# Optimization experiments

Hardware: AMD Instinct MI355X
Metric: run time of the kernel (lower is better)

## Reference

```python
import jax, jax.numpy as jnp
import numpy as np
import math

EPS = 1e-6
P_MIN = 1e-3
P_MAX = 10.0
NUM_ITERS = 3
REG = 1.0
K = 64       # num_clusters
D = 128      # cluster_dim
TOKEN = 256  # token_dim
B, N, C = 8, 8192, 512


def _l2norm(t):
    return t / jnp.clip(jnp.linalg.norm(t, axis=-1, keepdims=True), 1e-12)


def _mlp(h, W1, b1, W2, b2):
    # torch Linear: y = h @ W.T + b ; dropout is identity at eval
    return jax.nn.relu(h @ W1.T + b1) @ W2.T + b2


def _log_otp_solver(log_a, log_b, M, num_iters, reg):
    M = M / reg
    u = jnp.zeros_like(log_a)
    v = jnp.zeros_like(log_b)
    for _ in range(num_iters):  # fixed small iteration count
        u = log_a - jax.scipy.special.logsumexp(M + v[:, None, :], axis=2)
        v = log_b - jax.scipy.special.logsumexp(M + u[:, :, None], axis=1)
    return M + u[:, :, None] + v[:, None, :]


def _get_matching_probs(S, dustbin_score, num_iters, reg):
    b, m, n = S.shape
    dust_row = jnp.broadcast_to(dustbin_score, (b, 1, n)).astype(S.dtype)
    S_aug = jnp.concatenate([S, dust_row], axis=1)  # [b, m+1, n]
    norm = -math.log(n + m)
    log_a = jnp.full((m + 1,), norm, dtype=S.dtype).at[-1].add(math.log(n - m))
    log_a = jnp.broadcast_to(log_a, (b, m + 1))
    log_b = jnp.full((b, n), norm, dtype=S.dtype)
    log_P = _log_otp_solver(log_a, log_b, S_aug, num_iters, reg)
    return log_P - norm


def setup_inputs() -> dict:
    key = jax.random.key(0)
    ks = jax.random.split(key, 8)
    x = jax.random.normal(ks[0], (B, N, C), dtype=jnp.float32)

    def lin(k, fin, fout):
        k1, k2 = jax.random.split(k)
        W = 0.02 * jax.random.normal(k1, (fout, fin), dtype=jnp.float32)
        b = 0.02 * jax.random.normal(k2, (fout,), dtype=jnp.float32)
        return W, b

    tW1, tb1 = lin(ks[1], C, 512)
    tW2, tb2 = lin(ks[2], 512, TOKEN)
    cW1, cb1 = lin(ks[3], C, 512)
    cW2, cb2 = lin(ks[4], 512, D)
    sW1, sb1 = lin(ks[5], C, 512)
    sW2, sb2 = lin(ks[6], 512, K)
    # GeM p param init so that softplus(w)+p_min == 3.0
    gem_w = jnp.array([math.log(math.exp(3.0 - P_MIN) - 1.0)], dtype=jnp.float32)
    dust_bin = jnp.array(1.0, dtype=jnp.float32)
    return dict(x=x, gem_w=gem_w, dust_bin=dust_bin,
                tW1=tW1, tb1=tb1, tW2=tW2, tb2=tb2,
                cW1=cW1, cb1=cb1, cW2=cW2, cb2=cb2,
                sW1=sW1, sb1=sb1, sW2=sW2, sb2=sb2)


def reference(x, gem_w, dust_bin,
              tW1, tb1, tW2, tb2,
              cW1, cb1, cW2, cb2,
              sW1, sb1, sW2, sb2):
    # --- GeM pooling: [B, N, C] -> [B, C] ---
    p = jnp.minimum(jax.nn.softplus(gem_w) + P_MIN, P_MAX)  # [1]
    g = jnp.mean(jnp.clip(x.astype(jnp.float32), EPS, None) ** p, axis=1) ** (1.0 / p)
    g = jnp.where(jnp.isfinite(g), g, jnp.zeros_like(g))

    global_token = _mlp(g, tW1, tb1, tW2, tb2)          # [B, TOKEN]
    local = _mlp(x, cW1, cb1, cW2, cb2)                 # [B, N, D]
    scores = _mlp(x, sW1, sb1, sW2, sb2)                # [B, N, K]

    S = scores.transpose(0, 2, 1)                       # [B, K, N]
    log_P = _get_matching_probs(S, dust_bin, NUM_ITERS, REG)  # [B, K+1, N]
    p_mat = jnp.exp(log_P)[:, :-1, :]                   # drop dustbin -> [B, K, N]

    # aggregated[b, d, k] = sum_n local[b, n, d] * p[b, k, n]  (no O(B*D*K*N) blowup)
    agg = jnp.einsum('bnd,bkn->bdk', local, p_mat).reshape(x.shape[0], -1)  # [B, D*K]

    result = jnp.concatenate([_l2norm(global_token), _l2norm(agg)], axis=-1)
    return _l2norm(result)
```

## Files before the change

kernel.cpp:

```cpp
#include <hip/hip_runtime.h>
#include <hip/hip_bf16.h>
#include <math.h>

#define BB   8
#define NN   8192
#define CC   512
#define DD   128
#define KK   64
#define TOK  256
#define MM   (BB*NN)

typedef unsigned short u16;
typedef __attribute__((ext_vector_type(8))) short short8;
typedef __attribute__((ext_vector_type(4))) float floatx4;

struct PtrSz { const void* p[15]; int sz[15]; };

__device__ __forceinline__ float bf2f(u16 v) {
    union { unsigned u; float f; } x; x.u = ((unsigned)v) << 16; return x.f;
}
__device__ __forceinline__ u16 f2bf(float f) {
    union { float f; unsigned u; } x; x.f = f;
    unsigned r = x.u + 0x7fffu + ((x.u >> 16) & 1u);
    return (u16)(r >> 16);
}
__device__ __forceinline__ float nat_exp2(float a) {
    float r; asm("v_exp_f32 %0, %1" : "=v"(r) : "v"(a)); return r;
}
__device__ __forceinline__ float nat_log2(float a) {
    float r; asm("v_log_f32 %0, %1" : "=v"(r) : "v"(a)); return r;
}
__device__ __forceinline__ void gload16(const void* g, void* l) {
    __builtin_amdgcn_global_load_lds(
        (const __attribute__((address_space(1))) void*)g,
        (__attribute__((address_space(3))) void*)l, 16, 0, 0);
}

__global__ __launch_bounds__(256)
void fill_sentinel(float* __restrict__ out, int n, float val) {
    int i = blockIdx.x*256 + threadIdx.x;
    if (i < n) out[i] = val;
}

__global__ __launch_bounds__(256)
void detect_all(PtrSz ps, int* __restrict__ flags) {
    int i = blockIdx.x;
    const u16* q = (const u16*)ps.p[i];
    int m = ps.sz[i] < 4096 ? ps.sz[i] : 4096;
    __shared__ int cnt;
    if (threadIdx.x == 0) cnt = 0;
    __syncthreads();
    int c = 0;
    for (int j = threadIdx.x; j < m; j += 256) {
        int e = (q[j] >> 7) & 0xFF;
        if (e < 90 || e > 165) c++;
    }
    atomicAdd(&cnt, c);
    __syncthreads();
    if (threadIdx.x == 0) flags[i] = (cnt * 8 > m) ? 1 : 0;
}

#define W_TW1 0
#define W_TB1 262144
#define W_TW2 262656
#define W_TB2 393728
#define W_CW1 393984
#define W_CB1 656128
#define W_CW2 656640
#define W_CB2 722176
#define W_SW1 722304
#define W_SB1 984448
#define W_SW2 984960
#define W_SB2 1017728
#define W_TOTAL 1017792

__global__ __launch_bounds__(256)
void conv_weights(PtrSz ps, const int* __restrict__ flags,
                  u16* __restrict__ wbuf, float* __restrict__ wscal) {
    long gid = (long)blockIdx.x*256 + threadIdx.x;
    if (gid == 0) {
        float vb = bf2f(((const u16*)ps.p[1])[0]);
        float vf = ((const float*)ps.p[1])[0];
        wscal[0] = (fabsf(vb - 2.94694f) < 0.2f) ? vb : vf;
    } else if (gid == 1) {
        float vb = bf2f(((const u16*)ps.p[2])[0]);
        float vf = ((const float*)ps.p[2])[0];
        wscal[1] = (fabsf(vb - 1.0f) < 0.2f) ? vb : vf;
    }
    if (gid >= W_TOTAL) return;
    int idx; long off;
    if      (gid < W_TB1) { idx = 3;  off = W_TW1; }
    else if (gid < W_TW2) { idx = 4;  off = W_TB1; }
    else if (gid < W_TB2) { idx = 5;  off = W_TW2; }
    else if (gid < W_CW1) { idx = 6;  off = W_TB2; }
    else if (gid < W_CB1) { idx = 7;  off = W_CW1; }
    else if (gid < W_CW2) { idx = 8;  off = W_CB1; }
    else if (gid < W_CB2) { idx = 9;  off = W_CW2; }
    else if (gid < W_SW1) { idx = 10; off = W_CB2; }
    else if (gid < W_SB1) { idx = 11; off = W_SW1; }
    else if (gid < W_SW2) { idx = 12; off = W_SB1; }
    else if (gid < W_SB2) { idx = 13; off = W_SW2; }
    else                  { idx = 14; off = W_SB2; }
    long k = gid - off;
    bool f32in = flags[idx] != 0;
    wbuf[gid] = f32in ? f2bf(((const float*)ps.p[idx])[k]) : ((const u16*)ps.p[idx])[k];
}

__global__ __launch_bounds__(256)
void gem_partial(const void* __restrict__ x, const float* __restrict__ wscal,
                 const int* __restrict__ flags, float* __restrict__ gacc) {
    __shared__ float red[4][512];
    int b = blockIdx.x, ny = blockIdx.y;
    int tid  = threadIdx.x;
    int wave = tid >> 6, lane = tid & 63;
    bool f32in = (flags[0] != 0);
    float gw = wscal[0];
    float p  = fminf(log1pf(expf(gw)) + 1e-3f, 10.0f);
    int c0 = lane*8;
    float s[8];
#pragma unroll
    for (int j = 0; j < 8; ++j) s[j] = 0.f;
    size_t base = ((size_t)b*NN + (size_t)ny*64 + wave)*CC + c0;
    if (f32in) {
        const float* xf = (const float*)x;
#pragma unroll 4
        for (int n = 0; n < 64; n += 4) {
            const float* pf = xf + base + (size_t)n*CC;
            float4 x0 = *(const float4*)pf;
            float4 x1 = *(const float4*)(pf + 4);
            float xv[8] = {x0.x,x0.y,x0.z,x0.w,x1.x,x1.y,x1.z,x1.w};
#pragma unroll
            for (int j = 0; j < 8; ++j)
                s[j] += nat_exp2(p * nat_log2(fmaxf(xv[j], 1e-6f)));
        }
    } else {
        const u16* xu = (const u16*)x;
#pragma unroll 4
        for (int n = 0; n < 64; n += 4) {
            short8 v8 = *(const short8*)(xu + base + (size_t)n*CC);
#pragma unroll
            for (int j = 0; j < 8; ++j)
                s[j] += nat_exp2(p * nat_log2(fmaxf(bf2f((u16)v8[j]), 1e-6f)));
        }
    }
#pragma unroll
    for (int j = 0; j < 8; ++j) red[wave][c0 + j] = s[j];
    __syncthreads();
#pragma unroll
    for (int t = 0; t < 2; ++t) {
        int c = tid + t*256;
        float v = red[0][c] + red[1][c] + red[2][c] + red[3][c];
        atomicAdd(&gacc[b*CC + c], v);
    }
}

__global__ __launch_bounds__(256)
void gem_finalize(const float* __restrict__ gacc, const float* __restrict__ wscal,
                  float* __restrict__ g) {
    int i = blockIdx.x*256 + threadIdx.x;
    float gw = wscal[0];
    float p  = fminf(log1pf(expf(gw)) + 1e-3f, 10.0f);
    float m  = gacc[i] / (float)NN;
    float r  = powf(m, 1.0f/p);
    if (!isfinite(r)) r = 0.f;
    g[i] = r;
}

__global__ __launch_bounds__(512)
void token_mlp(const float* __restrict__ g, const u16* __restrict__ wbuf,
               float* __restrict__ t) {
    __shared__ float gs[CC];
    __shared__ float hs[512];
    int b = blockIdx.x, j = threadIdx.x;
    gs[j] = g[b*CC + j];
    __syncthreads();
    float a = bf2f(wbuf[W_TB1 + j]);
    const u16* w = wbuf + W_TW1 + (size_t)j*CC;
    for (int c = 0; c < CC; ++c) a += gs[c]*bf2f(w[c]);
    hs[j] = fmaxf(a, 0.f);
    __syncthreads();
    if (j < TOK) {
        float a2 = bf2f(wbuf[W_TB2 + j]);
        const u16* w2 = wbuf + W_TW2 + (size_t)j*512;
        for (int c = 0; c < 512; ++c) a2 += hs[c]*bf2f(w2[c]);
        t[b*TOK + j] = a2;
    }
}

template<int BN, int MODE, bool RELU, bool ARAW>
__global__ __launch_bounds__(256)
void gemm_bt(const void* __restrict__ A, const u16* __restrict__ W,
             const u16* __restrict__ bias, void* __restrict__ Cout,
             const int* __restrict__ flags, int N, int Ksz, int lda,
             size_t a_base, int bidx_ovr,
             const u16* __restrict__ W_alt, const u16* __restrict__ bias_alt,
             int nsplit) {
    constexpr int WSUB_N = BN/32;
    extern __shared__ char smem[];
    u16* a_lds = (u16*)smem;
    u16* b_lds = (u16*)smem + 128*32;
    const int tid  = threadIdx.x;
    const int wave = tid >> 6, lane = tid & 63;
    const int wm = wave >> 1, wn = wave & 1;

    int bx = blockIdx.x, by = blockIdx.y;
    {
        int nbx = gridDim.x, nby = gridDim.y;
        int nwg = nbx*nby;
        if ((nwg & 7) == 0) {
            int lid = bx + by*nbx;
            int q = nwg >> 3;
            int t = (lid & 7)*q + (lid >> 3);
            by = t % nby;
            bx = t / nby;
        }
    }
    const u16* Wp = W; const u16* bp = bias;
    int byw = by;
    if (W_alt != nullptr && by >= nsplit) { Wp = W_alt; bp = bias_alt; byw = by - nsplit; }
    const int bm0 = bx * 128;
    const int bn0 = by * BN;
    const int bw0 = byw * BN;
    const int fr = lane & 15;
    const int fk = (lane >> 4) * 8;
    const bool f32in = ARAW && (flags[0] != 0);

    floatx4 acc[4][WSUB_N];
#pragma unroll
    for (int i = 0; i < 4; ++i)
#pragma unroll
        for (int j = 0; j < WSUB_N; ++j) acc[i][j] = (floatx4){0.f,0.f,0.f,0.f};

    for (int k0 = 0; k0 < Ksz; k0 += 32) {
        if (f32in) {
#pragma unroll
            for (int part = 0; part < 2; ++part) {
                int chunk = part*256 + tid;
                int row = chunk >> 2, kc = (chunk & 3)*8;
                size_t gidx = a_base + (size_t)(bm0 + row)*lda + k0 + kc;
                const float* pf = (const float*)A + gidx;
                float4 x0 = *(const float4*)pf;
                float4 x1 = *(const float4*)(pf + 4);
                short8 vA;
                vA[0]=(short)f2bf(x0.x); vA[1]=(short)f2bf(x0.y);
                vA[2]=(short)f2bf(x0.z); vA[3]=(short)f2bf(x0.w);
                vA[4]=(short)f2bf(x1.x); vA[5]=(short)f2bf(x1.y);
                vA[6]=(short)f2bf(x1.z); vA[7]=(short)f2bf(x1.w);
                *(short8*)(a_lds + row*32 + kc) = vA;
            }
        } else {
#pragma unroll
            for (int part = 0; part < 2; ++part) {
                int cb = part*256 + wave*64;
                int mych = cb + lane;
                int row = mych >> 2, kc = (mych & 3)*8;
                gload16((const u16*)A + a_base + (size_t)(bm0 + row)*lda + k0 + kc,
                        a_lds + (size_t)cb*8);
            }
        }
#pragma unroll
        for (int part = 0; part < BN/64; ++part) {
            int cb = part*256 + wave*64;
            int mych = cb + lane;
            int row = mych >> 2, kc = (mych & 3)*8;
            gload16(Wp + (size_t)(bw0 + row)*Ksz + k0 + kc,
                    b_lds + (size_t)cb*8);
        }
        __syncthreads();
        short8 af[4], bfr[WSUB_N];
#pragma unroll
        for (int i = 0; i < 4; ++i)
            af[i] = *(const short8*)(a_lds + (wm*64 + i*16 + fr)*32 + fk);
#pragma unroll
        for (int j = 0; j < WSUB_N; ++j)
            bfr[j] = *(const short8*)(b_lds + (wn*WSUB_N*16 + j*16 + fr)*32 + fk);
#pragma unroll
        for (int i = 0; i < 4; ++i)
#pragma unroll
            for (int j = 0; j < WSUB_N; ++j)
                acc[i][j] = __builtin_amdgcn_mfma_f32_16x16x32_bf16(af[i], bfr[j], acc[i][j], 0, 0, 0);
        __syncthreads();
    }

    if constexpr (MODE == 0) {
        u16* C = (u16*)Cout;
#pragma unroll
        for (int i = 0; i < 4; ++i) {
            int row0 = wm*64 + i*16 + ((lane>>4)<<2);
#pragma unroll
            for (int j = 0; j < WSUB_N; ++j) {
                int col = wn*WSUB_N*16 + j*16 + fr;
                float bb = bf2f(bp[bw0+col]);
#pragma unroll
                for (int r = 0; r < 4; ++r) {
                    float v = acc[i][j][r] + bb;
                    if (RELU) v = fmaxf(v, 0.f);
                    C[(size_t)(bm0+row0+r)*N + (bn0+col)] = f2bf(v);
                }
            }
        }
    } else {
        const int bidx = (bidx_ovr >= 0) ? bidx_ovr : (bm0 >> 13);
        const int nin  = bm0 & 8191;
        if constexpr (MODE == 1) {
            u16* tr = (u16*)smem;
#pragma unroll
            for (int i = 0; i < 4; ++i) {
                int row0 = wm*64 + i*16 + ((lane>>4)<<2);
#pragma unroll
                for (int j = 0; j < WSUB_N; ++j) {
                    int col = wn*WSUB_N*16 + j*16 + fr;
                    float bb = bf2f(bp[bw0+col]);
#pragma unroll
                    for (int r = 0; r < 4; ++r) {
                        float v = acc[i][j][r] + bb;
                        if (RELU) v = fmaxf(v, 0.f);
                        tr[col*128 + row0 + r] = f2bf(v);
                    }
                }
            }
            __syncthreads();
            u16* O = (u16*)Cout;
#pragma unroll
            for (int c = 0; c < (BN*128)/256; ++c) {
                int flat = c*256 + tid;
                int dcol = flat >> 7, rr = flat & 127;
                O[(size_t)(bidx*BN + bn0 + dcol)*NN + nin + rr] = tr[dcol*128 + rr];
            }
        } else {
            float* tr = (float*)smem;
#pragma unroll
            for (int i = 0; i < 4; ++i) {
                int row0 = wm*64 + i*16 + ((lane>>4)<<2);
#pragma unroll
                for (int j = 0; j < WSUB_N; ++j) {
                    int col = wn*WSUB_N*16 + j*16 + fr;
                    float bb = bf2f(bp[bw0+col]);
#pragma unroll
                    for (int r = 0; r < 4; ++r) {
                        float v = acc[i][j][r] + bb;
                        if (RELU) v = fmaxf(v, 0.f);
                        tr[col*128 + row0 + r] = v;
                    }
                }
            }
            __syncthreads();
            float* O = (float*)Cout;
#pragma unroll
            for (int c = 0; c < (BN*128)/256; ++c) {
                int flat = c*256 + tid;
                int dcol = flat >> 7, rr = flat & 127;
                O[(size_t)(bidx*BN + bn0 + dcol)*NN + nin + rr] = tr[dcol*128 + rr];
            }
        }
    }
}

__global__ __launch_bounds__(256)
void sink_u(const float* __restrict__ ST, const float* __restrict__ v,
            const float* __restrict__ wscal, float* __restrict__ u) {
    int m = blockIdx.x, b = blockIdx.y, t = threadIdx.x;
    const float norm = -logf(8256.0f);
    float la = (m == 64) ? norm + logf(8128.0f) : norm;
    float dustf = wscal[1];
    const float* vb = v + (size_t)b*NN;
    float r[32];
    float mx = -1e30f;
    if (m < 64) {
        const float* row = ST + ((size_t)b*64 + m)*NN;
#pragma unroll
        for (int i = 0; i < 32; ++i) { int n = t + i*256; r[i] = row[n] + vb[n]; mx = fmaxf(mx, r[i]); }
    } else {
#pragma unroll
        for (int i = 0; i < 32; ++i) { int n = t + i*256; r[i] = dustf + vb[n]; mx = fmaxf(mx, r[i]); }
    }
#pragma unroll
    for (int off = 32; off; off >>= 1) mx = fmaxf(mx, __shfl_xor(mx, off));
    __shared__ float red[4];
    if ((t & 63) == 0) red[t>>6] = mx;
    __syncthreads();
    mx = fmaxf(fmaxf(red[0], red[1]), fmaxf(red[2], red[3]));
    __syncthreads();
    float s = 0.f;
#pragma unroll
    for (int i = 0; i < 32; ++i) s += expf(r[i] - mx);
#pragma unroll
    for (int off = 32; off; off >>= 1) s += __shfl_xor(s, off);
    if ((t & 63) == 0) red[t>>6] = s;
    __syncthreads();
    s = red[0] + red[1] + red[2] + red[3];
    if (t == 0) u[b*65 + m] = la - (mx + logf(s));
}

template<int WP>
__global__ __launch_bounds__(256)
void sink_v_t(const float* __restrict__ ST, const float* __restrict__ u,
              const float* __restrict__ wscal, float* __restrict__ v,
              u16* __restrict__ P) {
    int b = blockIdx.y;
    int n = blockIdx.x*256 + threadIdx.x;
    __shared__ float us[65];
    if (threadIdx.x < 65) us[threadIdx.x] = u[b*65 + threadIdx.x];
    __syncthreads();
    const float norm = -logf(8256.0f);
    float mx = wscal[1] + us[64];
    float s  = 1.0f;
    const float* col = ST + (size_t)b*64*NN + n;
    if (WP) {
        float r[64];
#pragma unroll
        for (int m = 0; m < 64; ++m) {
            r[m] = col[(size_t)m*NN] + us[m];
            float nm = fmaxf(mx, r[m]);
            s = s*expf(mx - nm) + expf(r[m] - nm);
            mx = nm;
        }
        float vn = norm - (mx + logf(s));
        v[(size_t)b*NN + n] = vn;
#pragma unroll
        for (int k = 0; k < 64; ++k)
            P[((size_t)b*64 + k)*NN + n] = f2bf(expf(r[k] + vn - norm));
    } else {
        for (int m = 0; m < 64; ++m) {
            float tv = col[(size_t)m*NN] + us[m];
            float nm = fmaxf(mx, tv);
            s = s*expf(mx - nm) + expf(tv - nm);
            mx = nm;
        }
        v[(size_t)b*NN + n] = norm - (mx + logf(s));
    }
}

__global__ __launch_bounds__(256)
void agg_mfma(const u16* __restrict__ localT, const u16* __restrict__ P,
              float* __restrict__ agg) {
    __shared__ u16 a_lds[128*32];
    __shared__ u16 b_lds[64*32];
    int b = blockIdx.y, ns = blockIdx.x;
    int n0 = ns*256;
    const int tid  = threadIdx.x;
    const int wave = tid >> 6, lane = tid & 63;
    const int wm = wave >> 1, wn = wave & 1;
    const int fr = lane & 15, fk = (lane >> 4)*8;

    floatx4 acc[4][2];
#pragma unroll
    for (int i = 0; i < 4; ++i)
#pragma unroll
        for (int j = 0; j < 2; ++j) acc[i][j] = (floatx4){0.f,0.f,0.f,0.f};

    for (int s = 0; s < 8; ++s) {
        int nk = n0 + s*32;
#pragma unroll
        for (int part = 0; part < 2; ++part) {
            int chunk = part*256 + tid;
            int row = chunk >> 2, kc = (chunk & 3)*8;
            short8 vA = *(const short8*)(localT + ((size_t)b*128 + row)*NN + nk + kc);
            *(short8*)(a_lds + row*32 + kc) = vA;
        }
        {
            int row = tid >> 2, kc = (tid & 3)*8;
            short8 vB = *(const short8*)(P + ((size_t)b*64 + row)*NN + nk + kc);
            *(short8*)(b_lds + row*32 + kc) = vB;
        }
        __syncthreads();
        short8 af[4], bfr[2];
#pragma unroll
        for (int i = 0; i < 4; ++i)
            af[i] = *(const short8*)(a_lds + (wm*64 + i*16 + fr)*32 + fk);
#pragma unroll
        for (int j = 0; j < 2; ++j)
            bfr[j] = *(const short8*)(b_lds + (wn*32 + j*16 + fr)*32 + fk);
#pragma unroll
        for (int i = 0; i < 4; ++i)
#pragma unroll
            for (int j = 0; j < 2; ++j)
                acc[i][j] = __builtin_amdgcn_mfma_f32_16x16x32_bf16(af[i], bfr[j], acc[i][j], 0, 0, 0);
        __syncthreads();
    }
#pragma unroll
    for (int i = 0; i < 4; ++i) {
        int d0 = wm*64 + i*16 + ((lane>>4)<<2);
#pragma unroll
        for (int j = 0; j < 2; ++j) {
            int k = wn*32 + j*16 + fr;
#pragma unroll
            for (int r = 0; r < 4; ++r)
                atomicAdd(&agg[(size_t)b*8192 + (d0+r)*64 + k], acc[i][j][r]);
        }
    }
}

__global__ __launch_bounds__(256)
void finalize_out(const float* __restrict__ tg, const float* __restrict__ agg,
                  float* __restrict__ out) {
    int b = blockIdx.x, tid = threadIdx.x;
    float tv = tg[b*TOK + tid];
    float s1 = tv*tv;
    const float* ab = agg + (size_t)b*8192;
    float av[32];
    float s2 = 0.f;
#pragma unroll
    for (int i = 0; i < 32; ++i) { av[i] = ab[tid + i*256]; s2 += av[i]*av[i]; }
#pragma unroll
    for (int off = 32; off; off >>= 1) { s1 += __shfl_xor(s1, off); s2 += __shfl_xor(s2, off); }
    __shared__ float r1[4], r2[4];
    int wave = tid >> 6, lane = tid & 63;
    if (lane == 0) { r1[wave] = s1; r2[wave] = s2; }
    __syncthreads();
    float S1 = r1[0]+r1[1]+r1[2]+r1[3];
    float S2 = r2[0]+r2[1]+r2[2]+r2[3];
    const float rs2 = 1.41421356237f;
    float sc1 = 1.0f/(fmaxf(sqrtf(S1), 1e-12f)*rs2);
    float sc2 = 1.0f/(fmaxf(sqrtf(S2), 1e-12f)*rs2);
    out[(size_t)b*8448 + tid] = tv*sc1;
#pragma unroll
    for (int i = 0; i < 32; ++i)
        out[(size_t)b*8448 + 256 + tid + i*256] = av[i]*sc2;
}

extern "C" void kernel_launch(void* const* d_in, const int* in_sizes, int n_in,
                              void* d_out, int out_size, void* d_ws, size_t ws_size,
                              hipStream_t stream) {
    float* out = (float*)d_out;

    static const int EXP[15] = {33554432,1,1,262144,512,131072,256,
                                262144,512,65536,128,262144,512,32768,64};
    bool ok = (n_in == 15) && (out_size == 67584);
    if (ok) for (int i = 0; i < 15; ++i) ok = ok && (in_sizes[i] == EXP[i]);
    if (!ok) {
        fill_sentinel<<<264, 256, 0, stream>>>(out, out_size, 0.25f);
        return;
    }
    const size_t NEED_BATCH = 52934656ull;
    if (ws_size < NEED_BATCH) {
        fill_sentinel<<<264, 256, 0, stream>>>(out, out_size, 0.5f);
        return;
    }

    const void* x = d_in[0];
    PtrSz ps;
    for (int i = 0; i < 15; ++i) { ps.p[i] = d_in[i]; ps.sz[i] = in_sizes[i]; }

    char* base = (char*)d_ws;
    float* gacc = (float*)(base + 0);
    float* u    = (float*)(base + 16384);
    float* v    = (float*)(base + 18464);
    float* agg  = (float*)(base + 280608);
    const size_t ZERO_BYTES = 542752;
    float* g    = (float*)(base + 542752);
    float* tglb = (float*)(base + 559136);
    int*   flags= (int*)  (base + 567328);
    float* wscal= (float*)(base + 567392);
    u16*   wbuf = (u16*)  (base + 567424);
    float* ST   = (float*)(base + 2603008);
    u16* localT = (u16*)  (base + 19380224);
    u16* P      = (u16*)  (base + 36157440);
    u16* h1     = (u16*)  (base + 44546048);
    const size_t FULL_NEED  = 44546048ull + 67108864ull;
    const size_t FUSED_NEED = 44546048ull + 134217728ull;
    const bool fused = (ws_size >= FUSED_NEED);
    const bool mono  = (ws_size >= FULL_NEED);

    hipMemsetAsync(d_ws, 0, ZERO_BYTES, stream);

    detect_all<<<15, 256, 0, stream>>>(ps, flags);
    conv_weights<<<3977, 256, 0, stream>>>(ps, flags, wbuf, wscal);

    gem_partial<<<dim3(BB, 128), 256, 0, stream>>>(x, wscal, flags, gacc);
    gem_finalize<<<16, 256, 0, stream>>>(gacc, wscal, g);
    token_mlp<<<BB, 512, 0, stream>>>(g, wbuf, tglb);

    const int NOSPLIT = 1 << 30;
    if (fused) {
        gemm_bt<128, 0, true,  true ><<<dim3(512, 8), 256, 16384, stream>>>(
            x, wbuf + W_CW1, wbuf + W_CB1, h1, flags, 1024, 512, 512, 0, -1,
            wbuf + W_SW1, wbuf + W_SB1, 4);
        gemm_bt<128, 1, false, false><<<dim3(512, 1), 256, 32768, stream>>>(
            h1, wbuf + W_CW2, wbuf + W_CB2, localT, flags, 128, 512, 1024, 0, -1,
            nullptr, nullptr, NOSPLIT);
        gemm_bt< 64, 2, false, false><<<dim3(512, 1), 256, 32768, stream>>>(
            h1, wbuf + W_SW2, wbuf + W_SB2, ST, flags, 64, 512, 1024, 512, -1,
            nullptr, nullptr, NOSPLIT);
    } else if (mono) {
        gemm_bt<128, 0, true,  true ><<<dim3(512, 4), 256, 16384, stream>>>(
            x, wbuf + W_CW1, wbuf + W_CB1, h1, flags, 512, 512, 512, 0, -1,
            nullptr, nullptr, NOSPLIT);
        gemm_bt<128, 1, false, false><<<dim3(512, 1), 256, 32768, stream>>>(
            h1, wbuf + W_CW2, wbuf + W_CB2, localT, flags, 128, 512, 512, 0, -1,
            nullptr, nullptr, NOSPLIT);
        gemm_bt<128, 0, true,  true ><<<dim3(512, 4), 256, 16384, stream>>>(
            x, wbuf + W_SW1, wbuf + W_SB1, h1, flags, 512, 512, 512, 0, -1,
            nullptr, nullptr, NOSPLIT);
        gemm_bt< 64, 2, false, false><<<dim3(512, 1), 256, 32768, stream>>>(
            h1, wbuf + W_SW2, wbuf + W_SB2, ST, flags, 64, 512, 512, 0, -1,
            nullptr, nullptr, NOSPLIT);
    } else {
        for (int b = 0; b < BB; ++b) {
            size_t ab = (size_t)b*NN*CC;
            gemm_bt<128, 0, true,  true ><<<dim3(64, 4), 256, 16384, stream>>>(
                x, wbuf + W_CW1, wbuf + W_CB1, h1, flags, 512, 512, 512, ab, -1,
                nullptr, nullptr, NOSPLIT);
            gemm_bt<128, 1, false, false><<<dim3(64, 1), 256, 32768, stream>>>(
                h1, wbuf + W_CW2, wbuf + W_CB2, localT, flags, 128, 512, 512, 0, b,
                nullptr, nullptr, NOSPLIT);
            gemm_bt<128, 0, true,  true ><<<dim3(64, 4), 256, 16384, stream>>>(
                x, wbuf + W_SW1, wbuf + W_SB1, h1, flags, 512, 512, 512, ab, -1,
                nullptr, nullptr, NOSPLIT);
            gemm_bt< 64, 2, false, false><<<dim3(64, 1), 256, 32768, stream>>>(
                h1, wbuf + W_SW2, wbuf + W_SB2, ST, flags, 64, 512, 512, 0, b,
                nullptr, nullptr, NOSPLIT);
        }
    }

    for (int it = 0; it < 3; ++it) {
        sink_u<<<dim3(65, BB), 256, 0, stream>>>(ST, v, wscal, u);
        if (it == 2)
            sink_v_t<1><<<dim3(32, BB), 256, 0, stream>>>(ST, u, wscal, v, P);
        else
            sink_v_t<0><<<dim3(32, BB), 256, 0, stream>>>(ST, u, wscal, v, P);
    }

    agg_mfma<<<dim3(32, BB), 256, 0, stream>>>(localT, P, agg);
    finalize_out<<<BB, 256, 0, stream>>>(tglb, agg, out);
}
```

Before: 514.3 us.

## Fuse Sinkhorn iterations into one cooperative kernel with grid sync

Replaces the six separate sink_u/sink_v launches with a single cooperative kernel. Each block keeps a 64x128 slice of the score matrix in LDS, writes per-slice partial max/sum for the row logsumexp, and uses grid.sync to combine them. The column logsumexp is then computed locally and P is written at the end. This removes repeated global reads of ST and the launch overhead, at the cost of grid-wide barriers and a fallback path if the cooperative launch fails. It also folds gem_finalize into token_mlp, saving one launch.

```diff
diff --git a/kernel.cpp b/kernel.cpp
--- a/kernel.cpp
+++ b/kernel.cpp
@@ -1,6 +1,9 @@
 #include <hip/hip_runtime.h>
 #include <hip/hip_bf16.h>
+#include <hip/hip_cooperative_groups.h>
 #include <math.h>
+
+namespace cg = cooperative_groups;
 
 #define BB   8
 #define NN   8192
@@ -154,25 +157,20 @@
     }
 }
 
-__global__ __launch_bounds__(256)
-void gem_finalize(const float* __restrict__ gacc, const float* __restrict__ wscal,
-                  float* __restrict__ g) {
-    int i = blockIdx.x*256 + threadIdx.x;
-    float gw = wscal[0];
-    float p  = fminf(log1pf(expf(gw)) + 1e-3f, 10.0f);
-    float m  = gacc[i] / (float)NN;
-    float r  = powf(m, 1.0f/p);
-    if (!isfinite(r)) r = 0.f;
-    g[i] = r;
-}
-
 __global__ __launch_bounds__(512)
-void token_mlp(const float* __restrict__ g, const u16* __restrict__ wbuf,
-               float* __restrict__ t) {
+void token_mlp(const float* __restrict__ gacc, const u16* __restrict__ wbuf,
+               const float* __restrict__ wscal, float* __restrict__ t) {
     __shared__ float gs[CC];
     __shared__ float hs[512];
     int b = blockIdx.x, j = threadIdx.x;
-    gs[j] = g[b*CC + j];
+    {
+        float gw = wscal[0];
+        float p  = fminf(log1pf(expf(gw)) + 1e-3f, 10.0f);
+        float m  = gacc[b*CC + j] / (float)NN;
+        float r  = powf(m, 1.0f/p);
+        if (!isfinite(r)) r = 0.f;
+        gs[j] = r;
+    }
     __syncthreads();
     float a = bf2f(wbuf[W_TB1 + j]);
     const u16* w = wbuf + W_TW1 + (size_t)j*CC;
@@ -356,6 +354,94 @@
     }
 }
 
+#define NSL 128
+__global__ __launch_bounds__(256)
+void sink_fused(const float* __restrict__ ST, const float* __restrict__ wscal,
+                u16* __restrict__ P, float* __restrict__ part) {
+    extern __shared__ char sm[];
+    float* Ssh = (float*)sm;
+    float* vsh = Ssh + 64*NSL;
+    float* us  = vsh + NSL;
+    const int g  = blockIdx.x;
+    const int b  = g >> 6, sl = g & 63;
+    const int n0 = sl*NSL;
+    const int t  = threadIdx.x;
+    const int wave = t >> 6, lane = t & 63;
+    const float norm = -logf(8256.0f);
+    const float L2E = 1.44269504089f, LN2 = 0.69314718056f;
+    const float dustf = wscal[1];
+
+    {
+        const float* src = ST + (size_t)b*64*NN + n0;
+        int r = t >> 5, c = (t & 31)*4;
+#pragma unroll
+        for (int i = 0; i < 8; ++i) {
+            int m = r + i*8;
+            *(float4*)(Ssh + m*NSL + c) = *(const float4*)(src + (size_t)m*NN + c);
+        }
+    }
+    if (t < NSL) vsh[t] = 0.f;
+    __syncthreads();
+
+    cg::grid_group grid = cg::this_grid();
+
+    for (int it = 0; it < 3; ++it) {
+        for (int m = wave; m < 65; m += 4) {
+            float v0, v1;
+            if (m < 64) {
+                v0 = Ssh[m*NSL + lane]      + vsh[lane];
+                v1 = Ssh[m*NSL + lane + 64] + vsh[lane + 64];
+            } else {
+                v0 = dustf + vsh[lane];
+                v1 = dustf + vsh[lane + 64];
+            }
+            float mx = fmaxf(v0, v1);
+#pragma unroll
+            for (int off = 32; off; off >>= 1) mx = fmaxf(mx, __shfl_xor(mx, off));
+            float s = nat_exp2((v0 - mx)*L2E) + nat_exp2((v1 - mx)*L2E);
+#pragma unroll
+            for (int off = 32; off; off >>= 1) s += __shfl_xor(s, off);
+            if (lane == 0) {
+                float2* pp = (float2*)part + ((size_t)(it*BB + b)*65 + m)*64 + sl;
+                *pp = make_float2(mx, s);
+            }
+        }
+        __threadfence();
+        grid.sync();
+        if (t < 65) {
+            const float2* pp = (const float2*)part + ((size_t)(it*BB + b)*65 + t)*64;
+            float gmx = -1e30f;
+            for (int i = 0; i < 64; ++i) gmx = fmaxf(gmx, pp[i].x);
+            float gs = 0.f;
+            for (int i = 0; i < 64; ++i) gs += pp[i].y * nat_exp2((pp[i].x - gmx)*L2E);
+            float la = (t == 64) ? norm + logf(8128.0f) : norm;
+            us[t] = la - (gmx + nat_log2(gs)*LN2);
+        }
+        __syncthreads();
+        if (t < NSL) {
+            float mx = dustf + us[64];
+            float s  = 1.0f;
+            for (int m = 0; m < 64; ++m) {
+                float tv = Ssh[m*NSL + t] + us[m];
+                float nm = fmaxf(mx, tv);
+                s = s*nat_exp2((mx - nm)*L2E) + nat_exp2((tv - nm)*L2E);
+                mx = nm;
+            }
+            vsh[t] = norm - (mx + nat_log2(s)*LN2);
+        }
+        __syncthreads();
+    }
+    {
+        int c = t & (NSL-1), h = t >> 7;
+        float vt = vsh[c];
+        u16* Pp = P + (size_t)b*64*NN + n0 + c;
+        for (int m = h*32; m < h*32 + 32; ++m) {
+            float lp = Ssh[m*NSL + c] + us[m] + vt - norm;
+            Pp[(size_t)m*NN] = f2bf(nat_exp2(lp*L2E));
+        }
+    }
+}
+
 __global__ __launch_bounds__(256)
 void sink_u(const float* __restrict__ ST, const float* __restrict__ v,
             const float* __restrict__ wscal, float* __restrict__ u) {
@@ -548,7 +634,6 @@
     float* v    = (float*)(base + 18464);
     float* agg  = (float*)(base + 280608);
     const size_t ZERO_BYTES = 542752;
-    float* g    = (float*)(base + 542752);
     float* tglb = (float*)(base + 559136);
     int*   flags= (int*)  (base + 567328);
     float* wscal= (float*)(base + 567392);
@@ -568,8 +653,7 @@
     conv_weights<<<3977, 256, 0, stream>>>(ps, flags, wbuf, wscal);
 
     gem_partial<<<dim3(BB, 128), 256, 0, stream>>>(x, wscal, flags, gacc);
-    gem_finalize<<<16, 256, 0, stream>>>(gacc, wscal, g);
-    token_mlp<<<BB, 512, 0, stream>>>(g, wbuf, tglb);
+    token_mlp<<<BB, 512, 0, stream>>>(gacc, wbuf, wscal, tglb);
 
     const int NOSPLIT = 1 << 30;
     if (fused) {
@@ -613,12 +697,22 @@
         }
     }
 
-    for (int it = 0; it < 3; ++it) {
-        sink_u<<<dim3(65, BB), 256, 0, stream>>>(ST, v, wscal, u);
-        if (it == 2)
-            sink_v_t<1><<<dim3(32, BB), 256, 0, stream>>>(ST, u, wscal, v, P);
-        else
-            sink_v_t<0><<<dim3(32, BB), 256, 0, stream>>>(ST, u, wscal, v, P);
+    {
+        const float* STa = ST; const float* wsa = wscal;
+        u16* Pa = P; float* parta = (float*)h1;
+        void* args[] = { (void*)&STa, (void*)&wsa, (void*)&Pa, (void*)&parta };
+        unsigned int lds = (64*NSL + NSL + 72) * 4;
+        hipError_t ce = hipLaunchCooperativeKernel(
+            (const void*)sink_fused, dim3(512), dim3(256), args, lds, stream);
+        if (ce != hipSuccess) {
+            for (int it = 0; it < 3; ++it) {
+                sink_u<<<dim3(65, BB), 256, 0, stream>>>(ST, v, wscal, u);
+                if (it == 2)
+                    sink_v_t<1><<<dim3(32, BB), 256, 0, stream>>>(ST, u, wscal, v, P);
+                else
+                    sink_v_t<0><<<dim3(32, BB), 256, 0, stream>>>(ST, u, wscal, v, P);
+            }
+        }
     }
 
     agg_mfma<<<dim3(32, BB), 256, 0, stream>>>(localT, P, agg);
```

Result: slower. 834.7 us (+62.3%).
